# Kernel optimization log

Measured on AMD Instinct MI355X. Metric: run time of the kernel, lower is better.

The kernel has to match this reference:

```python
import jax, jax.numpy as jnp
import numpy as np

N = 50000
E = 800000
D_IN = 384
D_H = 128
D_MLP = 128
K = 16


def layer_norm(x, g, b, eps=1e-5):
    m = x.mean(-1, keepdims=True)
    v = ((x - m) ** 2).mean(-1, keepdims=True)
    return (x - m) / jnp.sqrt(v + eps) * g + b


def setup_inputs() -> dict:
    key = jax.random.key(0)
    ks = jax.random.split(key, 16)
    s = lambda d: 1.0 / np.sqrt(d)
    return {
        "x": jax.random.normal(ks[0], (N, D_IN), jnp.float32),
        "edge_index": jax.random.randint(ks[1], (2, E), 0, N, jnp.int64),
        # GCNConv 1
        "W1": jax.random.normal(ks[2], (D_IN, D_H), jnp.float32) * s(D_IN),
        "b1": jnp.zeros((D_H,), jnp.float32),
        "g1": jnp.ones((D_H,), jnp.float32),
        "be1": jnp.zeros((D_H,), jnp.float32),
        # GCNConv 2
        "W2": jax.random.normal(ks[3], (D_H, D_H), jnp.float32) * s(D_H),
        "b2": jnp.zeros((D_H,), jnp.float32),
        "g2": jnp.ones((D_H,), jnp.float32),
        "be2": jnp.zeros((D_H,), jnp.float32),
        # residual projection (input_dim != conv_hidden)
        "rW": jax.random.normal(ks[4], (D_IN, D_H), jnp.float32) * s(D_IN),
        "rb": jnp.zeros((D_H,), jnp.float32),
        "rg": jnp.ones((D_H,), jnp.float32),
        "rbe": jnp.zeros((D_H,), jnp.float32),
        # MLP head
        "mW1": jax.random.normal(ks[5], (D_H, D_MLP), jnp.float32) * s(D_H),
        "mb1": jnp.zeros((D_MLP,), jnp.float32),
        "mg": jnp.ones((D_MLP,), jnp.float32),
        "mbe": jnp.zeros((D_MLP,), jnp.float32),
        "mW2": jax.random.normal(ks[6], (D_MLP, K), jnp.float32) * s(D_MLP),
        "mb2": jnp.zeros((K,), jnp.float32),
    }


def reference(x, edge_index, W1, b1, g1, be1, W2, b2, g2, be2,
              rW, rb, rg, rbe, mW1, mb1, mg, mbe, mW2, mb2):
    n = x.shape[0]
    loops = jnp.arange(n, dtype=edge_index.dtype)
    src = jnp.concatenate([edge_index[0], loops])  # [E+N]
    dst = jnp.concatenate([edge_index[1], loops])
    # symmetric GCN normalization with self-loops
    deg = jax.ops.segment_sum(jnp.ones_like(src, x.dtype), dst, num_segments=n)
    dinv = jnp.where(deg > 0, jax.lax.rsqrt(deg), 0.0)
    norm = dinv[src] * dinv[dst]  # [E+N]

    def gcn_conv(h, W, b):
        hw = h @ W  # [N, D_H]
        msg = hw[src] * norm[:, None]  # gather + scale, [E+N, D_H]
        return jax.ops.segment_sum(msg, dst, num_segments=n) + b

    # layer 1 with projected residual
    h = jax.nn.elu(layer_norm(gcn_conv(x, W1, b1), g1, be1))
    h = h + layer_norm(x @ rW + rb, rg, rbe)
    # layer 2 with identity residual
    h = jax.nn.elu(layer_norm(gcn_conv(h, W2, b2), g2, be2)) + h
    # MLP head (dropout inactive in eval) + softmax over clusters
    z = jax.nn.elu(layer_norm(h @ mW1 + mb1, mg, mbe))
    H = z @ mW2 + mb2
    return jax.nn.softmax(H, axis=1)
```

## Files before the change

### kernel.cpp

```cpp
#include <hip/hip_runtime.h>

#define DH 128

typedef __attribute__((ext_vector_type(8))) short short8;
typedef __attribute__((ext_vector_type(4))) float f32x4;

__device__ __forceinline__ float wave_sum(float v) {
    #pragma unroll
    for (int o = 32; o > 0; o >>= 1) v += __shfl_xor(v, o, 64);
    return v;
}

__device__ __forceinline__ void ln_pair(float v0, float v1, float& o0, float& o1) {
    float m = wave_sum(v0 + v1) * (1.f / 128.f);
    float d0 = v0 - m, d1 = v1 - m;
    float var = wave_sum(d0 * d0 + d1 * d1) * (1.f / 128.f);
    float inv = rsqrtf(var + 1e-5f);
    o0 = d0 * inv; o1 = d1 * inv;
}

__device__ __forceinline__ float elu(float x) { return x > 0.f ? x : expm1f(x); }

__device__ __forceinline__ unsigned short f2bf(float f) {
    unsigned u = __float_as_uint(f);
    u += 0x7fffu + ((u >> 16) & 1u);
    return (unsigned short)(u >> 16);
}
__device__ __forceinline__ float bfl(unsigned u) { return __uint_as_float(u << 16); }
__device__ __forceinline__ float bfh(unsigned u) { return __uint_as_float(u & 0xffff0000u); }
__device__ __forceinline__ unsigned pack_bf2(float a, float b) {
    return (unsigned)f2bf(a) | ((unsigned)f2bf(b) << 16);
}
__device__ __forceinline__ short8 cvt8(float4 v0, float4 v1) {
    short8 o;
    o[0] = (short)f2bf(v0.x); o[1] = (short)f2bf(v0.y);
    o[2] = (short)f2bf(v0.z); o[3] = (short)f2bf(v0.w);
    o[4] = (short)f2bf(v1.x); o[5] = (short)f2bf(v1.y);
    o[6] = (short)f2bf(v1.z); o[7] = (short)f2bf(v1.w);
    return o;
}

__global__ void zero_int_k(int* __restrict__ p, int n) {
    int i = blockIdx.x * 256 + threadIdx.x;
    if (i < n) p[i] = 0;
}

__global__ void deg_count_k(const int* __restrict__ dst, int* __restrict__ deg, int E) {
    int e = blockIdx.x * 256 + threadIdx.x;
    if (e < E) atomicAdd(&deg[dst[e]], 1);
}

__global__ void dinv_k(const int* __restrict__ deg, float* __restrict__ dinv, int n) {
    int i = blockIdx.x * 256 + threadIdx.x;
    if (i < n) dinv[i] = rsqrtf((float)(deg[i] + 1));
}

__global__ __launch_bounds__(1024) void scan_part_k(const int* __restrict__ deg,
                                                    int* __restrict__ rowptr,
                                                    int* __restrict__ bsum, int n)
{
    __shared__ int wsum[16];
    const int tid = threadIdx.x, lane = tid & 63, wid = tid >> 6;
    int i = blockIdx.x * 1024 + tid;
    int v = (i < n) ? deg[i] : 0;
    int s = v;
    #pragma unroll
    for (int o = 1; o < 64; o <<= 1) {
        int t = __shfl_up(s, o, 64);
        if (lane >= o) s += t;
    }
    if (lane == 63) wsum[wid] = s;
    __syncthreads();
    if (tid < 16) {
        int ws = wsum[tid];
        #pragma unroll
        for (int o = 1; o < 16; o <<= 1) {
            int t = __shfl_up(ws, o, 64);
            if (tid >= o) ws += t;
        }
        wsum[tid] = ws;
    }
    __syncthreads();
    int excl = (wid ? wsum[wid - 1] : 0) + s - v;
    if (i < n) rowptr[i] = excl;
    if (tid == 0) bsum[blockIdx.x] = wsum[15];
}

__global__ void scan_top_k(int* __restrict__ bsum, int* __restrict__ rowptr_n, int nb) {
    int lane = threadIdx.x;
    int carry = 0;
    for (int base = 0; base < nb; base += 64) {
        int i = base + lane;
        int v = (i < nb) ? bsum[i] : 0;
        int s = v;
        #pragma unroll
        for (int o = 1; o < 64; o <<= 1) {
            int t = __shfl_up(s, o, 64);
            if (lane >= o) s += t;
        }
        if (i < nb) bsum[i] = carry + s - v;
        carry += __shfl(s, 63, 64);
    }
    if (lane == 0) *rowptr_n = carry;
}

__global__ void scan_add_k(const int* __restrict__ bsum, int* __restrict__ rowptr,
                           int* __restrict__ cursor, int n)
{
    int i = blockIdx.x * 256 + threadIdx.x;
    if (i < n) {
        int v = rowptr[i] + bsum[i >> 10];
        rowptr[i] = v;
        cursor[i] = v;
    }
}

__global__ void fill_k(const int* __restrict__ src, const int* __restrict__ dst,
                       const float* __restrict__ dinv, int* __restrict__ cursor,
                       int2* __restrict__ csr, int E)
{
    int e = blockIdx.x * 256 + threadIdx.x;
    if (e < E) {
        int s = src[e], d = dst[e];
        float w = dinv[s] * dinv[d];
        int p = atomicAdd(&cursor[d], 1);
        csr[p] = make_int2(s, __float_as_int(w));
    }
}

__global__ void repack_w_k(const float* __restrict__ W, unsigned short* __restrict__ Wp, int K) {
    int idx = blockIdx.x * 256 + threadIdx.x;
    if (idx >= K * DH) return;
    int kb  = idx / (DH * 32);
    int rem = idx - kb * (DH * 32);
    int nn  = rem >> 5;
    int ki  = rem & 31;
    Wp[idx] = f2bf(W[(kb * 32 + ki) * DH + nn]);
}

template<int K, bool DUAL, bool AF32>
__global__ __launch_bounds__(256) void mfma_gemm(
    const void* __restrict__ Av,
    const unsigned short* __restrict__ Bp1, const float* __restrict__ ba,
    const unsigned short* __restrict__ Bp2, const float* __restrict__ bb,
    unsigned short* __restrict__ outa, unsigned short* __restrict__ outb, int n)
{
    constexpr int NKB = K / 32;
    const int tid = threadIdx.x;
    const int wid = tid >> 6, lane = tid & 63;
    const int m16 = lane & 15, q = lane >> 4;
    const long long rb0 = (long long)blockIdx.x * 128 + wid * 32;
    const int colb = blockIdx.y * 64;

    long long r0 = rb0 + m16;      if (r0 > (long long)n - 1) r0 = n - 1;
    long long r1 = rb0 + 16 + m16; if (r1 > (long long)n - 1) r1 = n - 1;

    const float* Af = (const float*)Av;
    const unsigned short* Ah = (const unsigned short*)Av;

    f32x4 acc1[2][4], acc2[2][4];
    const f32x4 zero = {0.f, 0.f, 0.f, 0.f};
    #pragma unroll
    for (int i = 0; i < 2; i++)
        #pragma unroll
        for (int j = 0; j < 4; j++) { acc1[i][j] = zero; if constexpr (DUAL) acc2[i][j] = zero; }

    float4 ra[2][2][2];
    short8 ha[2][2];
    short8 pb1[2][4], pb2[2][4];

    auto fetch = [&](int kb, int buf) {
        if constexpr (AF32) {
            const float* p0 = Af + r0 * K + kb * 32 + q * 8;
            const float* p1 = Af + r1 * K + kb * 32 + q * 8;
            ra[buf][0][0] = *(const float4*)p0;  ra[buf][0][1] = *(const float4*)(p0 + 4);
            ra[buf][1][0] = *(const float4*)p1;  ra[buf][1][1] = *(const float4*)(p1 + 4);
        } else {
            ha[buf][0] = *(const short8*)(Ah + r0 * K + kb * 32 + q * 8);
            ha[buf][1] = *(const short8*)(Ah + r1 * K + kb * 32 + q * 8);
        }
        #pragma unroll
        for (int nj = 0; nj < 4; ++nj) {
            long long boff = ((long long)kb * 128 + colb + nj * 16 + m16) * 32 + q * 8;
            pb1[buf][nj] = *(const short8*)(Bp1 + boff);
            if constexpr (DUAL) pb2[buf][nj] = *(const short8*)(Bp2 + boff);
        }
    };

    fetch(0, 0);
    #pragma unroll
    for (int kb = 0; kb < NKB; ++kb) {
        const int cur = kb & 1, nxt = cur ^ 1;
        if (kb + 1 < NKB) fetch(kb + 1, nxt);
        short8 af[2];
        if constexpr (AF32) {
            af[0] = cvt8(ra[cur][0][0], ra[cur][0][1]);
            af[1] = cvt8(ra[cur][1][0], ra[cur][1][1]);
        } else {
            af[0] = ha[cur][0];
            af[1] = ha[cur][1];
        }
        #pragma unroll
        for (int mi = 0; mi < 2; ++mi)
            #pragma unroll
            for (int nj = 0; nj < 4; ++nj) {
                acc1[mi][nj] = __builtin_amdgcn_mfma_f32_16x16x32_bf16(af[mi], pb1[cur][nj], acc1[mi][nj], 0, 0, 0);
                if constexpr (DUAL)
                    acc2[mi][nj] = __builtin_amdgcn_mfma_f32_16x16x32_bf16(af[mi], pb2[cur][nj], acc2[mi][nj], 0, 0, 0);
            }
    }

    #pragma unroll
    for (int nj = 0; nj < 4; ++nj) {
        int col = colb + nj * 16 + m16;
        float bav = ba ? ba[col] : 0.f;
        float bbv = 0.f;
        if constexpr (DUAL) bbv = bb ? bb[col] : 0.f;
        #pragma unroll
        for (int mi = 0; mi < 2; ++mi) {
            long long row0 = rb0 + mi * 16 + q * 4;
            #pragma unroll
            for (int r = 0; r < 4; ++r) {
                long long rr = row0 + r;
                if (rr < n) {
                    outa[rr * DH + col] = f2bf(acc1[mi][nj][r] + bav);
                    if constexpr (DUAL) outb[rr * DH + col] = f2bf(acc2[mi][nj][r] + bbv);
                }
            }
        }
    }
}

__device__ __forceinline__ void gather_row(
    const unsigned* __restrict__ hw, const int2* __restrict__ csr,
    int beg, int end, int lane, float& o0, float& o1)
{
    float a0 = 0.f, a1 = 0.f, b0 = 0.f, b1 = 0.f;
    float c0 = 0.f, c1 = 0.f, d0 = 0.f, d1 = 0.f;
    int p = beg;
    for (; p + 7 < end; p += 8) {
        int2 e0 = csr[p],     e1 = csr[p + 1], e2 = csr[p + 2], e3 = csr[p + 3];
        int2 e4 = csr[p + 4], e5 = csr[p + 5], e6 = csr[p + 6], e7 = csr[p + 7];
        unsigned u0 = hw[(long long)e0.x * 64 + lane];
        unsigned u1 = hw[(long long)e1.x * 64 + lane];
        unsigned u2 = hw[(long long)e2.x * 64 + lane];
        unsigned u3 = hw[(long long)e3.x * 64 + lane];
        unsigned u4 = hw[(long long)e4.x * 64 + lane];
        unsigned u5 = hw[(long long)e5.x * 64 + lane];
        unsigned u6 = hw[(long long)e6.x * 64 + lane];
        unsigned u7 = hw[(long long)e7.x * 64 + lane];
        float w0 = __int_as_float(e0.y), w1 = __int_as_float(e1.y);
        float w2 = __int_as_float(e2.y), w3 = __int_as_float(e3.y);
        float w4 = __int_as_float(e4.y), w5 = __int_as_float(e5.y);
        float w6 = __int_as_float(e6.y), w7 = __int_as_float(e7.y);
        a0 = fmaf(w0, bfl(u0), a0);  a1 = fmaf(w0, bfh(u0), a1);
        b0 = fmaf(w1, bfl(u1), b0);  b1 = fmaf(w1, bfh(u1), b1);
        c0 = fmaf(w2, bfl(u2), c0);  c1 = fmaf(w2, bfh(u2), c1);
        d0 = fmaf(w3, bfl(u3), d0);  d1 = fmaf(w3, bfh(u3), d1);
        a0 = fmaf(w4, bfl(u4), a0);  a1 = fmaf(w4, bfh(u4), a1);
        b0 = fmaf(w5, bfl(u5), b0);  b1 = fmaf(w5, bfh(u5), b1);
        c0 = fmaf(w6, bfl(u6), c0);  c1 = fmaf(w6, bfh(u6), c1);
        d0 = fmaf(w7, bfl(u7), d0);  d1 = fmaf(w7, bfh(u7), d1);
    }
    for (; p + 3 < end; p += 4) {
        int2 e0 = csr[p], e1 = csr[p + 1], e2 = csr[p + 2], e3 = csr[p + 3];
        unsigned u0 = hw[(long long)e0.x * 64 + lane];
        unsigned u1 = hw[(long long)e1.x * 64 + lane];
        unsigned u2 = hw[(long long)e2.x * 64 + lane];
        unsigned u3 = hw[(long long)e3.x * 64 + lane];
        float w0 = __int_as_float(e0.y), w1 = __int_as_float(e1.y);
        float w2 = __int_as_float(e2.y), w3 = __int_as_float(e3.y);
        a0 = fmaf(w0, bfl(u0), a0);  a1 = fmaf(w0, bfh(u0), a1);
        b0 = fmaf(w1, bfl(u1), b0);  b1 = fmaf(w1, bfh(u1), b1);
        c0 = fmaf(w2, bfl(u2), c0);  c1 = fmaf(w2, bfh(u2), c1);
        d0 = fmaf(w3, bfl(u3), d0);  d1 = fmaf(w3, bfh(u3), d1);
    }
    for (; p < end; ++p) {
        int2 e0 = csr[p];
        unsigned u0 = hw[(long long)e0.x * 64 + lane];
        float w0 = __int_as_float(e0.y);
        a0 = fmaf(w0, bfl(u0), a0);
        a1 = fmaf(w0, bfh(u0), a1);
    }
    o0 = (a0 + b0) + (c0 + d0);
    o1 = (a1 + b1) + (c1 + d1);
}

__global__ __launch_bounds__(256) void gfuse1_k(
    const unsigned* __restrict__ hw, const unsigned* __restrict__ proj,
    const int* __restrict__ rowptr, const int2* __restrict__ csr,
    const float* __restrict__ dinv,
    const float* __restrict__ b1, const float* __restrict__ g1, const float* __restrict__ be1,
    const float* __restrict__ rg, const float* __restrict__ rbe,
    unsigned* __restrict__ hout, int n)
{
    int row = blockIdx.x * 4 + (threadIdx.x >> 6);
    if (row >= n) return;
    int lane = threadIdx.x & 63;
    float a0, a1;
    gather_row(hw, csr, rowptr[row], rowptr[row + 1], lane, a0, a1);
    long long off = (long long)row * 64;
    float di = dinv[row], sl = di * di;
    unsigned us = hw[off + lane];
    float2 bv  = *(const float2*)(b1 + 2 * lane);
    float2 gv  = *(const float2*)(g1 + 2 * lane);
    float2 bev = *(const float2*)(be1 + 2 * lane);
    float2 rgv = *(const float2*)(rg + 2 * lane);
    float2 rbv = *(const float2*)(rbe + 2 * lane);
    float v0 = a0 + sl * bfl(us) + bv.x;
    float v1 = a1 + sl * bfh(us) + bv.y;
    float o0, o1; ln_pair(v0, v1, o0, o1);
    float t0 = elu(o0 * gv.x + bev.x);
    float t1 = elu(o1 * gv.y + bev.y);
    unsigned up = proj[off + lane];
    float q0, q1; ln_pair(bfl(up), bfh(up), q0, q1);
    hout[off + lane] = pack_bf2(t0 + q0 * rgv.x + rbv.x, t1 + q1 * rgv.y + rbv.y);
}

__global__ __launch_bounds__(256) void gfuse2_k(
    const unsigned* __restrict__ hw, const unsigned* __restrict__ hprev,
    const int* __restrict__ rowptr, const int2* __restrict__ csr,
    const float* __restrict__ dinv,
    const float* __restrict__ b2, const float* __restrict__ g2, const float* __restrict__ be2,
    unsigned* __restrict__ h2, int n)
{
    int row = blockIdx.x * 4 + (threadIdx.x >> 6);
    if (row >= n) return;
    int lane = threadIdx.x & 63;
    float a0, a1;
    gather_row(hw, csr, rowptr[row], rowptr[row + 1], lane, a0, a1);
    long long off = (long long)row * 64;
    float di = dinv[row], sl = di * di;
    unsigned us = hw[off + lane];
    float2 bv  = *(const float2*)(b2 + 2 * lane);
    float2 gv  = *(const float2*)(g2 + 2 * lane);
    float2 bev = *(const float2*)(be2 + 2 * lane);
    float v0 = a0 + sl * bfl(us) + bv.x;
    float v1 = a1 + sl * bfh(us) + bv.y;
    float o0, o1; ln_pair(v0, v1, o0, o1);
    float t0 = elu(o0 * gv.x + bev.x);
    float t1 = elu(o1 * gv.y + bev.y);
    unsigned uh = hprev[off + lane];
    h2[off + lane] = pack_bf2(t0 + bfl(uh), t1 + bfh(uh));
}

__global__ __launch_bounds__(256) void head_k(
    const unsigned* __restrict__ zraw, const float* __restrict__ g, const float* __restrict__ be,
    const float* __restrict__ mW2, const float* __restrict__ mb2,
    float* __restrict__ out, int n)
{
    int row = blockIdx.x * 4 + (threadIdx.x >> 6);
    if (row >= n) return;
    int lane = threadIdx.x & 63;
    unsigned u = zraw[(long long)row * 64 + lane];
    float o0, o1; ln_pair(bfl(u), bfh(u), o0, o1);
    float2 gv  = *(const float2*)(g + 2 * lane);
    float2 bev = *(const float2*)(be + 2 * lane);
    float z0 = elu(o0 * gv.x + bev.x);
    float z1 = elu(o1 * gv.y + bev.y);
    int k = lane & 15, seg = lane >> 4;
    float acc = 0.f;
    #pragma unroll
    for (int t = 0; t < 16; ++t) {
        int srcl = seg * 16 + t;
        float zz0 = __shfl(z0, srcl, 64);
        float zz1 = __shfl(z1, srcl, 64);
        int c = seg * 32 + 2 * t;
        acc = fmaf(zz0, mW2[c * 16 + k], acc);
        acc = fmaf(zz1, mW2[(c + 1) * 16 + k], acc);
    }
    acc += __shfl_xor(acc, 32, 64);
    acc += __shfl_xor(acc, 16, 64);
    float hk = acc + mb2[k];
    float mx = hk;
    #pragma unroll
    for (int o = 8; o > 0; o >>= 1) mx = fmaxf(mx, __shfl_xor(mx, o, 64));
    float e = expf(hk - mx);
    float s = e;
    #pragma unroll
    for (int o = 8; o > 0; o >>= 1) s += __shfl_xor(s, o, 64);
    if (lane < 16) out[(long long)row * 16 + k] = e / s;
}

static inline size_t align16(size_t x) { return (x + 15) & ~(size_t)15; }

extern "C" void kernel_launch(void* const* d_in, const int* in_sizes, int n_in,
                              void* d_out, int out_size, void* d_ws, size_t ws_size,
                              hipStream_t stream)
{
    const float* x   = (const float*)d_in[0];
    const int*   ei  = (const int*)d_in[1];
    const float* W1  = (const float*)d_in[2];
    const float* b1  = (const float*)d_in[3];
    const float* g1  = (const float*)d_in[4];
    const float* be1 = (const float*)d_in[5];
    const float* W2  = (const float*)d_in[6];
    const float* b2  = (const float*)d_in[7];
    const float* g2  = (const float*)d_in[8];
    const float* be2 = (const float*)d_in[9];
    const float* rW  = (const float*)d_in[10];
    const float* rb  = (const float*)d_in[11];
    const float* rg  = (const float*)d_in[12];
    const float* rbe = (const float*)d_in[13];
    const float* mW1 = (const float*)d_in[14];
    const float* mb1 = (const float*)d_in[15];
    const float* mg  = (const float*)d_in[16];
    const float* mbe = (const float*)d_in[17];
    const float* mW2 = (const float*)d_in[18];
    const float* mb2 = (const float*)d_in[19];
    float* out = (float*)d_out;

    const int n = in_sizes[0] / 384;
    const int E = in_sizes[1] / 2;
    const int* src = ei;
    const int* dst = ei + E;

    char* w = (char*)d_ws;
    int* deg     = (int*)w;   w += align16((size_t)n * 4);
    int* rowptr  = (int*)w;   w += align16((size_t)(n + 1) * 4);
    int* cursor  = (int*)w;   w += align16((size_t)n * 4);
    float* dinv  = (float*)w; w += align16((size_t)n * 4);
    int* bsum    = (int*)w;   w += align16((size_t)1024 * 4);
    int2* csr    = (int2*)w;  w += align16((size_t)E * 8);
    unsigned short* hw1  = (unsigned short*)w; w += align16((size_t)n * DH * 2);
    unsigned short* proj = (unsigned short*)w; w += align16((size_t)n * DH * 2);
    unsigned short* hbuf = (unsigned short*)w; w += align16((size_t)n * DH * 2);
    unsigned short* Wp1 = (unsigned short*)w; w += align16((size_t)384 * DH * 2);
    unsigned short* Wpr = (unsigned short*)w; w += align16((size_t)384 * DH * 2);
    unsigned short* Wp2 = (unsigned short*)w; w += align16((size_t)128 * DH * 2);
    unsigned short* WpM = (unsigned short*)w; w += align16((size_t)128 * DH * 2);
    unsigned short* hw2  = hw1;
    unsigned short* h2   = proj;
    unsigned short* zraw = hbuf;

    int gE = (E + 255) / 256;
    int gN = (n + 255) / 256;
    int nb = (n + 1023) / 1024;
    dim3 gG((n + 127) / 128, 2);
    int gRow4 = (n + 3) / 4;

    zero_int_k<<<gN, 256, 0, stream>>>(deg, n);
    deg_count_k<<<gE, 256, 0, stream>>>(dst, deg, E);
    dinv_k<<<gN, 256, 0, stream>>>(deg, dinv, n);
    scan_part_k<<<nb, 1024, 0, stream>>>(deg, rowptr, bsum, n);
    scan_top_k<<<1, 64, 0, stream>>>(bsum, rowptr + n, nb);
    scan_add_k<<<gN, 256, 0, stream>>>(bsum, rowptr, cursor, n);
    fill_k<<<gE, 256, 0, stream>>>(src, dst, dinv, cursor, csr, E);

    repack_w_k<<<(384 * DH + 255) / 256, 256, 0, stream>>>(W1, Wp1, 384);
    repack_w_k<<<(384 * DH + 255) / 256, 256, 0, stream>>>(rW, Wpr, 384);
    repack_w_k<<<(128 * DH + 255) / 256, 256, 0, stream>>>(W2, Wp2, 128);
    repack_w_k<<<(128 * DH + 255) / 256, 256, 0, stream>>>(mW1, WpM, 128);

    mfma_gemm<384, true, true><<<gG, 256, 0, stream>>>(x, Wp1, nullptr, Wpr, rb, hw1, proj, n);
    gfuse1_k<<<gRow4, 256, 0, stream>>>((unsigned*)hw1, (unsigned*)proj, rowptr, csr, dinv,
                                        b1, g1, be1, rg, rbe, (unsigned*)hbuf, n);

    mfma_gemm<128, false, false><<<gG, 256, 0, stream>>>(hbuf, Wp2, nullptr, nullptr, nullptr, hw2, nullptr, n);
    gfuse2_k<<<gRow4, 256, 0, stream>>>((unsigned*)hw2, (unsigned*)hbuf, rowptr, csr, dinv,
                                        b2, g2, be2, (unsigned*)h2, n);

    mfma_gemm<128, false, false><<<gG, 256, 0, stream>>>(h2, WpM, mb1, nullptr, nullptr, zraw, nullptr, n);
    head_k<<<gRow4, 256, 0, stream>>>((unsigned*)zraw, mg, mbe, mW2, mb2, out, n);
}
```

Baseline: 449.4 us.

## Pre-convert x to bf16 and triple-buffer A loads in MFMA GEMM

Adds a separate pass that converts the fp32 input x to bf16 once, so the first GEMM reads half-width A rows. Since the grid has two column blocks, each reading the full x, this halves that GEMM's A traffic but adds a full read of x plus a write and re-read of a bf16 copy. The GEMM drops its fp32 path and prefetches A two k-blocks ahead with a three-slot buffer to hide load latency. The four weight-repack launches are merged into one kernel writing one contiguous buffer, which removes launch overhead.

```diff
diff --git a/kernel.cpp b/kernel.cpp
--- a/kernel.cpp
+++ b/kernel.cpp
@@ -40,6 +40,19 @@
     return o;
 }
 
+__global__ __launch_bounds__(256) void conv_x_k(const float* __restrict__ x,
+                                                unsigned short* __restrict__ xb,
+                                                long long n8)
+{
+    long long i = (long long)blockIdx.x * 256 + threadIdx.x;
+    long long stride = (long long)gridDim.x * 256;
+    for (; i < n8; i += stride) {
+        float4 v0 = *(const float4*)(x + i * 8);
+        float4 v1 = *(const float4*)(x + i * 8 + 4);
+        *(short8*)(xb + i * 8) = cvt8(v0, v1);
+    }
+}
+
 __global__ void zero_int_k(int* __restrict__ p, int n) {
     int i = blockIdx.x * 256 + threadIdx.x;
     if (i < n) p[i] = 0;
@@ -128,19 +141,26 @@
     }
 }
 
-__global__ void repack_w_k(const float* __restrict__ W, unsigned short* __restrict__ Wp, int K) {
+__global__ void repack_all_k(const float* __restrict__ W1, const float* __restrict__ rW,
+                             const float* __restrict__ W2, const float* __restrict__ mW1,
+                             unsigned short* __restrict__ Wp)
+{
     int idx = blockIdx.x * 256 + threadIdx.x;
-    if (idx >= K * DH) return;
-    int kb  = idx / (DH * 32);
-    int rem = idx - kb * (DH * 32);
-    int nn  = rem >> 5;
-    int ki  = rem & 31;
+    if (idx >= 131072) return;
+    const float* W; int base;
+    if (idx < 49152)       { W = W1;  base = 0; }
+    else if (idx < 98304)  { W = rW;  base = 49152; }
+    else if (idx < 114688) { W = W2;  base = 98304; }
+    else                   { W = mW1; base = 114688; }
+    int l = idx - base;
+    int kb = l >> 12, rem = l & 4095;
+    int nn = rem >> 5, ki = rem & 31;
     Wp[idx] = f2bf(W[(kb * 32 + ki) * DH + nn]);
 }
 
-template<int K, bool DUAL, bool AF32>
+template<int K, bool DUAL>
 __global__ __launch_bounds__(256) void mfma_gemm(
-    const void* __restrict__ Av,
+    const unsigned short* __restrict__ A,
     const unsigned short* __restrict__ Bp1, const float* __restrict__ ba,
     const unsigned short* __restrict__ Bp2, const float* __restrict__ bb,
     unsigned short* __restrict__ outa, unsigned short* __restrict__ outb, int n)
@@ -155,9 +175,6 @@
     long long r0 = rb0 + m16;      if (r0 > (long long)n - 1) r0 = n - 1;
     long long r1 = rb0 + 16 + m16; if (r1 > (long long)n - 1) r1 = n - 1;
 
-    const float* Af = (const float*)Av;
-    const unsigned short* Ah = (const unsigned short*)Av;
-
     f32x4 acc1[2][4], acc2[2][4];
     const f32x4 zero = {0.f, 0.f, 0.f, 0.f};
     #pragma unroll
@@ -165,20 +182,14 @@
         #pragma unroll
         for (int j = 0; j < 4; j++) { acc1[i][j] = zero; if constexpr (DUAL) acc2[i][j] = zero; }
 
-    float4 ra[2][2][2];
-    short8 ha[2][2];
+    short8 ha[3][2];
     short8 pb1[2][4], pb2[2][4];
 
-    auto fetch = [&](int kb, int buf) {
-        if constexpr (AF32) {
-            const float* p0 = Af + r0 * K + kb * 32 + q * 8;
-            const float* p1 = Af + r1 * K + kb * 32 + q * 8;
-            ra[buf][0][0] = *(const float4*)p0;  ra[buf][0][1] = *(const float4*)(p0 + 4);
-            ra[buf][1][0] = *(const float4*)p1;  ra[buf][1][1] = *(const float4*)(p1 + 4);
-        } else {
-            ha[buf][0] = *(const short8*)(Ah + r0 * K + kb * 32 + q * 8);
-            ha[buf][1] = *(const short8*)(Ah + r1 * K + kb * 32 + q * 8);
-        }
+    auto fetchA = [&](int kb, int buf) {
+        ha[buf][0] = *(const short8*)(A + r0 * K + kb * 32 + q * 8);
+        ha[buf][1] = *(const short8*)(A + r1 * K + kb * 32 + q * 8);
+    };
+    auto fetchB = [&](int kb, int buf) {
         #pragma unroll
         for (int nj = 0; nj < 4; ++nj) {
             long long boff = ((long long)kb * 128 + colb + nj * 16 + m16) * 32 + q * 8;
@@ -187,26 +198,22 @@
         }
     };
 
-    fetch(0, 0);
+    fetchA(0, 0);
+    fetchB(0, 0);
+    if constexpr (NKB > 1) fetchA(1, 1);
+
     #pragma unroll
     for (int kb = 0; kb < NKB; ++kb) {
-        const int cur = kb & 1, nxt = cur ^ 1;
-        if (kb + 1 < NKB) fetch(kb + 1, nxt);
-        short8 af[2];
-        if constexpr (AF32) {
-            af[0] = cvt8(ra[cur][0][0], ra[cur][0][1]);
-            af[1] = cvt8(ra[cur][1][0], ra[cur][1][1]);
-        } else {
-            af[0] = ha[cur][0];
-            af[1] = ha[cur][1];
-        }
+        if (kb + 2 < NKB) fetchA(kb + 2, (kb + 2) % 3);
+        if (kb + 1 < NKB) fetchB(kb + 1, (kb + 1) & 1);
+        const int ca = kb % 3, cb = kb & 1;
         #pragma unroll
         for (int mi = 0; mi < 2; ++mi)
             #pragma unroll
             for (int nj = 0; nj < 4; ++nj) {
-                acc1[mi][nj] = __builtin_amdgcn_mfma_f32_16x16x32_bf16(af[mi], pb1[cur][nj], acc1[mi][nj], 0, 0, 0);
+                acc1[mi][nj] = __builtin_amdgcn_mfma_f32_16x16x32_bf16(ha[ca][mi], pb1[cb][nj], acc1[mi][nj], 0, 0, 0);
                 if constexpr (DUAL)
-                    acc2[mi][nj] = __builtin_amdgcn_mfma_f32_16x16x32_bf16(af[mi], pb2[cur][nj], acc2[mi][nj], 0, 0, 0);
+                    acc2[mi][nj] = __builtin_amdgcn_mfma_f32_16x16x32_bf16(ha[ca][mi], pb2[cb][nj], acc2[mi][nj], 0, 0, 0);
             }
     }
 
@@ -422,13 +429,15 @@
     float* dinv  = (float*)w; w += align16((size_t)n * 4);
     int* bsum    = (int*)w;   w += align16((size_t)1024 * 4);
     int2* csr    = (int2*)w;  w += align16((size_t)E * 8);
+    unsigned short* xb   = (unsigned short*)w; w += align16((size_t)n * 384 * 2);
     unsigned short* hw1  = (unsigned short*)w; w += align16((size_t)n * DH * 2);
     unsigned short* proj = (unsigned short*)w; w += align16((size_t)n * DH * 2);
     unsigned short* hbuf = (unsigned short*)w; w += align16((size_t)n * DH * 2);
-    unsigned short* Wp1 = (unsigned short*)w; w += align16((size_t)384 * DH * 2);
-    unsigned short* Wpr = (unsigned short*)w; w += align16((size_t)384 * DH * 2);
-    unsigned short* Wp2 = (unsigned short*)w; w += align16((size_t)128 * DH * 2);
-    unsigned short* WpM = (unsigned short*)w; w += align16((size_t)128 * DH * 2);
+    unsigned short* Wp   = (unsigned short*)w; w += align16((size_t)131072 * 2);
+    unsigned short* Wp1 = Wp;
+    unsigned short* Wpr = Wp + 49152;
+    unsigned short* Wp2 = Wp + 98304;
+    unsigned short* WpM = Wp + 114688;
     unsigned short* hw2  = hw1;
     unsigned short* h2   = proj;
     unsigned short* zraw = hbuf;
@@ -438,6 +447,9 @@
     int nb = (n + 1023) / 1024;
     dim3 gG((n + 127) / 128, 2);
     int gRow4 = (n + 3) / 4;
+
+    conv_x_k<<<2048, 256, 0, stream>>>(x, xb, (long long)n * 48);
+    repack_all_k<<<512, 256, 0, stream>>>(W1, rW, W2, mW1, Wp);
 
     zero_int_k<<<gN, 256, 0, stream>>>(deg, n);
     deg_count_k<<<gE, 256, 0, stream>>>(dst, deg, E);
@@ -447,19 +459,14 @@
     scan_add_k<<<gN, 256, 0, stream>>>(bsum, rowptr, cursor, n);
     fill_k<<<gE, 256, 0, stream>>>(src, dst, dinv, cursor, csr, E);
 
-    repack_w_k<<<(384 * DH + 255) / 256, 256, 0, stream>>>(W1, Wp1, 384);
-    repack_w_k<<<(384 * DH + 255) / 256, 256, 0, stream>>>(rW, Wpr, 384);
-    repack_w_k<<<(128 * DH + 255) / 256, 256, 0, stream>>>(W2, Wp2, 128);
-    repack_w_k<<<(128 * DH + 255) / 256, 256, 0, stream>>>(mW1, WpM, 128);
-
-    mfma_gemm<384, true, true><<<gG, 256, 0, stream>>>(x, Wp1, nullptr, Wpr, rb, hw1, proj, n);
+    mfma_gemm<384, true><<<gG, 256, 0, stream>>>(xb, Wp1, nullptr, Wpr, rb, hw1, proj, n);
     gfuse1_k<<<gRow4, 256, 0, stream>>>((unsigned*)hw1, (unsigned*)proj, rowptr, csr, dinv,
                                         b1, g1, be1, rg, rbe, (unsigned*)hbuf, n);
 
-    mfma_gemm<128, false, false><<<gG, 256, 0, stream>>>(hbuf, Wp2, nullptr, nullptr, nullptr, hw2, nullptr, n);
+    mfma_gemm<128, false><<<gG, 256, 0, stream>>>(hbuf, Wp2, nullptr, nullptr, nullptr, hw2, nullptr, n);
     gfuse2_k<<<gRow4, 256, 0, stream>>>((unsigned*)hw2, (unsigned*)hbuf, rowptr, csr, dinv,
                                         b2, g2, be2, (unsigned*)h2, n);
 
-    mfma_gemm<128, false, false><<<gG, 256, 0, stream>>>(h2, WpM, mb1, nullptr, nullptr, zraw, nullptr, n);
+    mfma_gemm<128, false><<<gG, 256, 0, stream>>>(h2, WpM, mb1, nullptr, nullptr, zraw, nullptr, n);
     head_k<<<gRow4, 256, 0, stream>>>((unsigned*)zraw, mg, mbe, mW2, mb2, out, n);
 }
```

Result: no change. 456.6 us (+1.6%).
